# Performance work log

Hardware: AMD Instinct MI355X
Metric: run time of the kernel (lower is better)

Reference implementation:

```python
import jax, jax.numpy as jnp
import numpy as np
import math

N, E, D, R, L = 20000, 640000, 128, 16, 3
R_MAX = math.sqrt(2.0)
CENTERS = jnp.linspace(0.0, R_MAX, R)          # GaussianRBF centers on [0, sqrt(2)]
GAMMA = 1.0 / (2.0 * (R_MAX / (R - 1)) ** 2)   # 1/(2*sigma^2), sigma = center spacing


def _mlp(x, w1, b1, w2, b2):
    # mlp([din, d_h, dout]): Linear -> SiLU -> Linear (dropout=0.0)
    return jax.nn.silu(x @ w1 + b1) @ w2 + b2


def _ln(x, g, b):
    mu = jnp.mean(x, axis=-1, keepdims=True)
    v = jnp.var(x, axis=-1, keepdims=True)
    return (x - mu) * jax.lax.rsqrt(v + 1e-5) * g + b


def _time_emb(t):
    # SinusoidalEmbedding(dim=D)
    half = D // 2
    freqs = jnp.exp(-math.log(10000.0) * jnp.arange(half, dtype=jnp.float32) / (half - 1))
    a = t * freqs
    return jnp.concatenate([jnp.sin(a), jnp.cos(a)])


def setup_inputs():
    key = jax.random.key(0)
    ks = jax.random.split(key, 16)
    s = 0.05
    p = {}
    p["x_t"] = jax.random.normal(ks[0], (N, 3), dtype=jnp.float32)
    p["edge_index"] = jax.random.randint(ks[1], (2, E), 0, N)
    p["t"] = 25
    p["time_w1"] = jax.random.normal(ks[2], (D, D)) * s
    p["time_b1"] = jnp.zeros((D,))
    p["time_w2"] = jax.random.normal(ks[3], (D, D)) * s
    p["time_b2"] = jnp.zeros((D,))
    p["nodein_w1"] = jax.random.normal(ks[4], (3 + D, D)) * s
    p["nodein_b1"] = jnp.zeros((D,))
    p["nodein_w2"] = jax.random.normal(ks[5], (D, D)) * s
    p["nodein_b2"] = jnp.zeros((D,))
    p["phim_w1"] = jax.random.normal(ks[6], (L, 2 * D + R, D)) * s
    p["phim_b1"] = jnp.zeros((L, D))
    p["phim_w2"] = jax.random.normal(ks[7], (L, D, D)) * s
    p["phim_b2"] = jnp.zeros((L, D))
    p["phih_w1"] = jax.random.normal(ks[8], (L, 2 * D, D)) * s
    p["phih_b1"] = jnp.zeros((L, D))
    p["phih_w2"] = jax.random.normal(ks[9], (L, D, D)) * s
    p["phih_b2"] = jnp.zeros((L, D))
    p["ln_g"] = jnp.ones((L, D))
    p["ln_b"] = jnp.zeros((L, D))
    p["out_w1"] = jax.random.normal(ks[10], (D, D)) * s
    p["out_b1"] = jnp.zeros((D,))
    p["out_w2"] = jax.random.normal(ks[11], (D, 3)) * s
    p["out_b2"] = jnp.zeros((3,))
    return p


def reference(x_t, edge_index, t,
              time_w1, time_b1, time_w2, time_b2,
              nodein_w1, nodein_b1, nodein_w2, nodein_b2,
              phim_w1, phim_b1, phim_w2, phim_b2,
              phih_w1, phih_b1, phih_w2, phih_b2,
              ln_g, ln_b,
              out_w1, out_b1, out_w2, out_b2):
    # GraphDenoiser.forward: one denoiser call of the diffusion sampling loop.
    n = x_t.shape[0]
    src, dst = edge_index[0], edge_index[1]

    te = _mlp(_time_emb(jnp.asarray(t, jnp.float32)), time_w1, time_b1, time_w2, time_b2)
    h = _mlp(jnp.concatenate([x_t, jnp.broadcast_to(te, (n, D))], axis=-1),
             nodein_w1, nodein_b1, nodein_w2, nodein_b2)

    # edge geometry is fixed across layers (depends only on x_t)
    dx = x_t[src, :2] - x_t[dst, :2]                     # [E, 2]
    r = jnp.sqrt(jnp.sum(dx * dx, axis=-1) + 1e-8)       # [E]
    rbf = jnp.exp(-GAMMA * (r[:, None] - CENTERS) ** 2)  # [E, R]

    for i in range(L):  # WeightedInvariantMPNNLayer x L (edge_weight == 1)
        m_in = jnp.concatenate([h[src], h[dst], rbf], axis=-1)      # [E, 2D+R]
        m = _mlp(m_in, phim_w1[i], phim_b1[i], phim_w2[i], phim_b2[i])
        agg = jax.ops.segment_sum(m, dst, num_segments=n)           # scatter_sum
        h_up = _mlp(jnp.concatenate([h, agg], axis=-1),
                    phih_w1[i], phih_b1[i], phih_w2[i], phih_b2[i])
        h = _ln(h + h_up, ln_g[i], ln_b[i])

    return _mlp(h, out_w1, out_b1, out_w2, out_b2)  # predicted eps, [N, 3]
```

## Files before the change

### kernel.cpp

```cpp
#include <hip/hip_runtime.h>

typedef unsigned short u16;
typedef unsigned int u32;

#define NNODES 20000
#define NEDGES 640000
#define RBF_GAMMA 56.25f
#define SQRT2 1.4142135623730951f
#define PITCH 132
#define BPITCH 136

typedef __bf16 bf16x8 __attribute__((ext_vector_type(8)));
typedef float f32x4 __attribute__((ext_vector_type(4)));

__device__ __forceinline__ float b2f(u16 u) {
    union { float f; u32 i; } x; x.i = ((u32)u) << 16; return x.f;
}
__device__ __forceinline__ float hi2f(u32 w) {
    union { float f; u32 i; } x; x.i = w & 0xffff0000u; return x.f;
}
__device__ __forceinline__ float lo2f(u32 w) {
    union { float f; u32 i; } x; x.i = w << 16; return x.f;
}
__device__ __forceinline__ u16 f2b(float f) {
    union { float f; u32 i; } x; x.f = f;
    u32 r = (x.i + 0x7fffu + ((x.i >> 16) & 1u)) >> 16;
    return (u16)r;
}
__device__ __forceinline__ float silu(float v) {
    return v * __builtin_amdgcn_rcpf(1.0f + __expf(-v));
}
__device__ __forceinline__ void fma4(float4 w, float4 s, float& acc) {
    acc = fmaf(w.x, s.x, acc);
    acc = fmaf(w.y, s.y, acc);
    acc = fmaf(w.z, s.z, acc);
    acc = fmaf(w.w, s.w, acc);
}

__global__ __launch_bounds__(256) void k_hist(const int* __restrict__ ei, int* __restrict__ hist) {
    int e = blockIdx.x * 256 + threadIdx.x;
    atomicAdd(&hist[ei[NEDGES + e]], 1);
}

__global__ __launch_bounds__(1024) void k_scan(const int* __restrict__ hist,
                                               int* __restrict__ row_ptr,
                                               int* __restrict__ cursor) {
    __shared__ int psum[1024];
    int t = threadIdx.x;
    int base = t * 20;
    int s = 0;
    if (base < NNODES)
        for (int i = 0; i < 20; ++i) s += hist[base + i];
    psum[t] = s;
    __syncthreads();
    for (int off = 1; off < 1024; off <<= 1) {
        int v = (t >= off) ? psum[t - off] : 0;
        __syncthreads();
        psum[t] += v;
        __syncthreads();
    }
    int excl = psum[t] - s;
    if (base < NNODES) {
        int run = excl;
        for (int i = 0; i < 20; ++i) {
            row_ptr[base + i] = run;
            cursor[base + i] = run;
            run += hist[base + i];
        }
    }
    if (t == 1023) row_ptr[NNODES] = psum[1023];
}

__global__ __launch_bounds__(256) void k_scatter(const int* __restrict__ ei, int* __restrict__ cursor,
                                                 int* __restrict__ ssrc, int* __restrict__ sdst) {
    int e = blockIdx.x * 256 + threadIdx.x;
    int d = ei[NEDGES + e];
    int pos = atomicAdd(&cursor[d], 1);
    ssrc[pos] = ei[e];
    sdst[pos] = d;
}

__global__ __launch_bounds__(256) void k_prep_wr(const float* __restrict__ pmw1,
                                                 const float* __restrict__ pmb1,
                                                 u16* __restrict__ Wr) {
    int id = blockIdx.x * 256 + threadIdx.x;
    if (id >= 1536) return;
    int l = id / 512; int r = id - l * 512;
    int nt = r >> 6, lane = r & 63;
    int col = nt * 16 + (lane & 15);
    alignas(16) u16 tmp[8];
    #pragma unroll
    for (int jj = 0; jj < 8; ++jj) {
        int kk = (lane >> 4) * 8 + jj;
        float v = 0.f;
        if (kk < 16) v = pmw1[l * 34816 + (256 + kk) * 128 + col];
        else if (kk == 16) v = pmb1[l * 128 + col];
        tmp[jj] = f2b(v);
    }
    *(uint4*)(Wr + (size_t)id * 8) = *(const uint4*)tmp;
}

__global__ __launch_bounds__(256) void k_prep_yw(const float* __restrict__ pmw1,
                                                 u16* __restrict__ Yw) {
    int id = blockIdx.x * 256 + threadIdx.x;
    if (id >= 12288) return;
    int lane = id & 63;
    int g = id >> 6;
    int nt = g & 7; g >>= 3;
    int kc = g & 3; g >>= 2;
    int mat = g & 1; int l = g >> 1;
    int col = nt * 16 + (lane & 15);
    int kb = kc * 32 + ((lane >> 4) & 3) * 8;
    alignas(16) u16 tmp[8];
    #pragma unroll
    for (int jj = 0; jj < 8; ++jj)
        tmp[jj] = f2b(pmw1[(size_t)l * 34816 + (mat * 128 + kb + jj) * 128 + col]);
    *(uint4*)(Yw + (size_t)id * 8) = *(const uint4*)tmp;
}

struct PackM { const float* s[11]; float* d[11]; int K[11]; };
__global__ __launch_bounds__(256) void k_pack(PackM pm) {
    int m = blockIdx.y;
    int idx = blockIdx.x * 256 + threadIdx.x;
    if (idx >= pm.K[m] * 128) return;
    int k = idx >> 7, j = idx & 127;
    pm.d[m][(k >> 2) * 512 + j * 4 + (k & 3)] = pm.s[m][idx];
}

__global__ __launch_bounds__(256) void k_prep_m(const float* __restrict__ pmw2,
        const float* __restrict__ pmb2, const float* __restrict__ V1p,
        float* __restrict__ Mp, float* __restrict__ bvv) {
    const int l = blockIdx.y, bx = blockIdx.x;
    const float* V1 = V1p + (size_t)l * 32768;
    const int tid = threadIdx.x;
    const int w = tid >> 6, lane = tid & 63;
    const int cg = lane & 15, ng = lane >> 4;
    const int jc0 = w * 32 + cg * 2, jc1 = jc0 + 1;
    __shared__ alignas(16) float W2L[16][PITCH];
    __shared__ float b2L[128];
    if (bx < 8) {
        const float4* src = (const float4*)(pmw2 + (size_t)l * 16384 + bx * 16 * 128);
        for (int q = tid; q < 512; q += 256) {
            int row = q >> 5, part = q & 31;
            *(float4*)&W2L[row][part * 4] = src[q];
        }
        __syncthreads();
        int r0 = ng * 4;
        float acc[4][2];
        #pragma unroll
        for (int n = 0; n < 4; ++n) { acc[n][0] = 0.f; acc[n][1] = 0.f; }
        for (int mm = 0; mm < 32; ++mm) {
            float4 wa = *(const float4*)(V1 + (32 + mm) * 512 + jc0 * 4);
            float4 wb = *(const float4*)(V1 + (32 + mm) * 512 + jc1 * 4);
            #pragma unroll
            for (int n = 0; n < 4; ++n) {
                float4 s4 = *(const float4*)&W2L[r0 + n][mm * 4];
                fma4(wa, s4, acc[n][0]);
                fma4(wb, s4, acc[n][1]);
            }
        }
        #pragma unroll
        for (int n = 0; n < 4; ++n) {
            int kg = bx * 16 + r0 + n;
            Mp[(size_t)l * 16384 + (kg >> 2) * 512 + jc0 * 4 + (kg & 3)] = acc[n][0];
            Mp[(size_t)l * 16384 + (kg >> 2) * 512 + jc1 * 4 + (kg & 3)] = acc[n][1];
        }
    } else {
        if (tid < 128) b2L[tid] = pmb2[l * 128 + tid];
        __syncthreads();
        if (ng == 0) {
            float a0 = 0.f, a1 = 0.f;
            for (int mm = 0; mm < 32; ++mm) {
                float4 wa = *(const float4*)(V1 + (32 + mm) * 512 + jc0 * 4);
                float4 wb = *(const float4*)(V1 + (32 + mm) * 512 + jc1 * 4);
                float4 s4 = *(const float4*)&b2L[mm * 4];
                fma4(wa, s4, a0);
                fma4(wb, s4, a1);
            }
            bvv[l * 128 + jc0] = a0;
            bvv[l * 128 + jc1] = a1;
        }
    }
}

__global__ __launch_bounds__(128) void k_time(const int* __restrict__ tptr,
        const float* __restrict__ tw1, const float* __restrict__ tb1,
        const float* __restrict__ tw2, const float* __restrict__ tb2,
        const float* __restrict__ nw1, const float* __restrict__ nb1,
        float* __restrict__ base1) {
    __shared__ float emb[128], hid[128], te[128];
    int j = threadIdx.x;
    int raw = tptr[0];
    float tv;
    if (raw >= 0 && raw < (1 << 24)) tv = (float)raw;
    else tv = __int_as_float(raw);
    float fr = expf(-9.210340371976184f * (float)(j & 63) / 63.0f);
    float a = tv * fr;
    emb[j] = (j < 64) ? sinf(a) : cosf(a);
    __syncthreads();
    float acc = tb1[j];
    for (int k = 0; k < 128; ++k) acc += emb[k] * tw1[k * 128 + j];
    hid[j] = silu(acc);
    __syncthreads();
    acc = tb2[j];
    for (int k = 0; k < 128; ++k) acc += hid[k] * tw2[k * 128 + j];
    te[j] = acc;
    __syncthreads();
    acc = nb1[j];
    for (int k = 0; k < 128; ++k) acc += te[k] * nw1[(3 + k) * 128 + j];
    base1[j] = acc;
}

__global__ __launch_bounds__(256) void k_h0(const float* __restrict__ x, const float* __restrict__ base1,
        const float* __restrict__ nw1, const float* __restrict__ nw2p, const float* __restrict__ nb2,
        const u16* __restrict__ Yw,
        float* __restrict__ hf, u16* __restrict__ Ysrc, u16* __restrict__ Ydst) {
    const int tid = threadIdx.x;
    const int w = tid >> 6, lane = tid & 63;
    const int cg = lane & 15, ng = lane >> 4;
    const int jc0 = w * 32 + cg * 2, jc1 = jc0 + 1;
    const int n0 = ng * 4;
    const int base = blockIdx.x * 16;
    __shared__ alignas(16) float xl[16][4];
    __shared__ alignas(16) float hid[16][PITCH];
    __shared__ alignas(16) u16 hb16[16 * BPITCH];
    if (tid < 48) { int n = tid / 3, cc = tid - n * 3; xl[n][cc] = x[(size_t)(base + n) * 3 + cc]; }
    __syncthreads();
    {
        float w0a = nw1[jc0], w0b = nw1[jc1];
        float w1a = nw1[128 + jc0], w1b = nw1[128 + jc1];
        float w2a = nw1[256 + jc0], w2b = nw1[256 + jc1];
        float ba = base1[jc0], bb = base1[jc1];
        #pragma unroll
        for (int n = 0; n < 4; ++n) {
            int row = n0 + n;
            float x0 = xl[row][0], x1 = xl[row][1], x2 = xl[row][2];
            float2 v;
            v.x = silu(ba + x0 * w0a + x1 * w1a + x2 * w2a);
            v.y = silu(bb + x0 * w0b + x1 * w1b + x2 * w2b);
            *(float2*)&hid[row][jc0] = v;
        }
    }
    __syncthreads();
    float acc[4][2];
    {
        float ba = nb2[jc0], bb = nb2[jc1];
        #pragma unroll
        for (int n = 0; n < 4; ++n) { acc[n][0] = ba; acc[n][1] = bb; }
        for (int kk = 0; kk < 32; ++kk) {
            float4 wa = *(const float4*)(nw2p + kk * 512 + jc0 * 4);
            float4 wb = *(const float4*)(nw2p + kk * 512 + jc1 * 4);
            #pragma unroll
            for (int n = 0; n < 4; ++n) {
                float4 s4 = *(const float4*)&hid[n0 + n][kk * 4];
                fma4(wa, s4, acc[n][0]);
                fma4(wb, s4, acc[n][1]);
            }
        }
    }
    __syncthreads();
    #pragma unroll
    for (int n = 0; n < 4; ++n) {
        int row = n0 + n;
        *(float2*)&hf[(size_t)(base + row) * 128 + jc0] = make_float2(acc[n][0], acc[n][1]);
        *(u32*)&hb16[row * BPITCH + jc0] = (u32)f2b(acc[n][0]) | ((u32)f2b(acc[n][1]) << 16);
    }
    __syncthreads();
    {
        const int mat = w >> 1, half = w & 1;
        const int lrow = lane & 15, quad = lane >> 4;
        bf16x8 a[4];
        #pragma unroll
        for (int kc = 0; kc < 4; ++kc)
            a[kc] = *(const bf16x8*)(hb16 + lrow * BPITCH + kc * 32 + quad * 8);
        u16* dst = mat ? Ydst : Ysrc;
        #pragma unroll
        for (int t = 0; t < 4; ++t) {
            int nt = half * 4 + t;
            f32x4 a4 = {0.f, 0.f, 0.f, 0.f};
            #pragma unroll
            for (int kc = 0; kc < 4; ++kc) {
                bf16x8 b = *(const bf16x8*)(Yw + (size_t)(((mat * 4 + kc) * 8 + nt) * 512 + lane * 8));
                a4 = __builtin_amdgcn_mfma_f32_16x16x32_bf16(a[kc], b, a4, 0, 0, 0);
            }
            #pragma unroll
            for (int r = 0; r < 4; ++r)
                dst[(size_t)(base + quad * 4 + r) * 128 + nt * 16 + lrow] = f2b(a4[r]);
        }
    }
}

__global__ __launch_bounds__(512, 8) void k_edge(
        const u16* __restrict__ Ysrc, const u16* __restrict__ Ydst,
        const float* __restrict__ x,
        const int* __restrict__ ssrc, const int* __restrict__ sdst,
        const u16* __restrict__ Wr,
        float* __restrict__ s_glob) {
    __shared__ alignas(16) u16 sst[128 * 72];
    __shared__ alignas(16) u16 ys[64 * 128];
    __shared__ float rv[64];
    __shared__ int s_d[65];
    __shared__ int s_s[64];
    const int tid = threadIdx.x;
    const int e0 = blockIdx.x * 64;
    if (tid < 64) {
        int s = ssrc[e0 + tid], d = sdst[e0 + tid];
        s_s[tid] = s; s_d[tid] = d;
        float ddx = x[s * 3] - x[d * 3];
        float ddy = x[s * 3 + 1] - x[d * 3 + 1];
        rv[tid] = sqrtf(ddx * ddx + ddy * ddy + 1e-8f);
    } else if (tid == 64) {
        s_d[64] = -1;
    }
    __syncthreads();
    #pragma unroll
    for (int i = 0; i < 2; ++i) {
        int cch = tid + i * 512;
        int e = cch >> 4, part = cch & 15;
        *(uint4*)(ys + e * 128 + part * 8) = *(const uint4*)(Ysrc + (size_t)s_s[e] * 128 + part * 8);
    }
    const int w = tid >> 6, lane = tid & 63;
    const int m = w & 3, nh = w >> 2;
    const int lrow = lane & 15, quad = lane >> 4;
    float r = rv[m * 16 + lrow];
    union { bf16x8 v; u16 u[8]; } af;
    #pragma unroll
    for (int j = 0; j < 8; ++j) {
        int kk = quad * 8 + j;
        float v;
        if (kk < 16) {
            float dd = r - SQRT2 * (float)kk / 15.0f;
            v = __expf(-RBF_GAMMA * dd * dd);
        } else v = (kk == 16) ? 1.0f : 0.0f;
        af.u[j] = f2b(v);
    }
    {
        const u16* Bp = Wr + lane * 8;
        #pragma unroll
        for (int t = 0; t < 4; ++t) {
            int nt = nh * 4 + t;
            f32x4 a4 = {0.f, 0.f, 0.f, 0.f};
            bf16x8 b = *(const bf16x8*)(Bp + nt * 512);
            a4 = __builtin_amdgcn_mfma_f32_16x16x32_bf16(af.v, b, a4, 0, 0, 0);
            int col = nt * 16 + lrow;
            u32 lo = (u32)f2b(a4[0]) | ((u32)f2b(a4[1]) << 16);
            u32 hi = (u32)f2b(a4[2]) | ((u32)f2b(a4[3]) << 16);
            *(uint2*)(sst + col * 72 + m * 16 + quad * 4) = make_uint2(lo, hi);
        }
    }
    __syncthreads();
    {
        const int col = tid & 127, q = tid >> 7;
        const int r0 = q * 16;
        float a = 0.f;
        int cd = s_d[r0];
        float yd = b2f(Ydst[(size_t)cd * 128 + col]);
        #pragma unroll
        for (int h = 0; h < 2; ++h) {
            uint4 c0 = *(const uint4*)(sst + col * 72 + r0 + h * 8);
            float sv8[8];
            sv8[0] = lo2f(c0.x); sv8[1] = hi2f(c0.x);
            sv8[2] = lo2f(c0.y); sv8[3] = hi2f(c0.y);
            sv8[4] = lo2f(c0.z); sv8[5] = hi2f(c0.z);
            sv8[6] = lo2f(c0.w); sv8[7] = hi2f(c0.w);
            #pragma unroll
            for (int i = 0; i < 8; ++i) {
                int rr = r0 + h * 8 + i;
                int nd = s_d[rr + 1];
                float v = sv8[i] + b2f(ys[rr * 128 + col]) + yd;
                a += silu(v);
                bool last = (h == 1 && i == 7);
                if (last || nd != cd) {
                    atomicAdd(&s_glob[(size_t)cd * 128 + col], a);
                    a = 0.f;
                    if (!last && nd != cd)
                        yd = b2f(Ydst[(size_t)nd * 128 + col]);
                }
                cd = nd;
            }
        }
    }
}

__global__ __launch_bounds__(256) void k_node(float* __restrict__ s_glob, const int* __restrict__ row_ptr,
        float* __restrict__ hf,
        const float* __restrict__ Mp, const float* __restrict__ V1p, const float* __restrict__ V2p,
        const float* __restrict__ bv, const float* __restrict__ c1, const float* __restrict__ c2,
        const float* __restrict__ lng, const float* __restrict__ lnb,
        const u16* __restrict__ Yw,
        u16* __restrict__ Ysrc, u16* __restrict__ Ydst) {
    const int tid = threadIdx.x;
    const int w = tid >> 6, lane = tid & 63;
    const int cg = lane & 15, ng = lane >> 4;
    const int jc0 = w * 32 + cg * 2, jc1 = jc0 + 1;
    const int n0 = ng * 4;
    const int base = blockIdx.x * 16;
    __shared__ alignas(16) float sv[16][PITCH], hv[16][PITCH];
    __shared__ alignas(16) u16 ybf[16 * BPITCH];
    __shared__ float mv[16][2];
    __shared__ int rp[17];
    float (*uv)[PITCH] = sv;
    float (*xs)[PITCH] = sv;

    if (tid < 17) rp[tid] = row_ptr[base + tid];
    {
        const float4* sg4 = (const float4*)(s_glob + (size_t)base * 128);
        float4* sg4w = (float4*)(s_glob + (size_t)base * 128);
        const float4* hg4 = (const float4*)(hf + (size_t)base * 128);
        for (int q = tid; q < 512; q += 256) {
            int row = q >> 5, part = q & 31;
            *(float4*)&sv[row][part * 4] = sg4[q];
            *(float4*)&hv[row][part * 4] = hg4[q];
            sg4w[q] = make_float4(0.f, 0.f, 0.f, 0.f);
        }
    }
    __syncthreads();

    float acc[4][2];
    {
        float ba = c1[jc0], bb = c1[jc1];
        float bva = bv[jc0], bvb = bv[jc1];
        #pragma unroll
        for (int n = 0; n < 4; ++n) {
            float dg = (float)(rp[n0 + n + 1] - rp[n0 + n]);
            acc[n][0] = ba + dg * bva; acc[n][1] = bb + dg * bvb;
        }
        for (int kk = 0; kk < 32; ++kk) {
            float4 wa = *(const float4*)(V1p + kk * 512 + jc0 * 4);
            float4 wb = *(const float4*)(V1p + kk * 512 + jc1 * 4);
            #pragma unroll
            for (int n = 0; n < 4; ++n) {
                float4 s4 = *(const float4*)&hv[n0 + n][kk * 4];
                fma4(wa, s4, acc[n][0]);
                fma4(wb, s4, acc[n][1]);
            }
        }
        for (int kk = 0; kk < 32; ++kk) {
            float4 wa = *(const float4*)(Mp + kk * 512 + jc0 * 4);
            float4 wb = *(const float4*)(Mp + kk * 512 + jc1 * 4);
            #pragma unroll
            for (int n = 0; n < 4; ++n) {
                float4 s4 = *(const float4*)&sv[n0 + n][kk * 4];
                fma4(wa, s4, acc[n][0]);
                fma4(wb, s4, acc[n][1]);
            }
        }
    }
    __syncthreads();
    #pragma unroll
    for (int n = 0; n < 4; ++n)
        *(float2*)&uv[n0 + n][jc0] = make_float2(silu(acc[n][0]), silu(acc[n][1]));
    __syncthreads();
    {
        float ba = c2[jc0], bb = c2[jc1];
        #pragma unroll
        for (int n = 0; n < 4; ++n) { acc[n][0] = ba; acc[n][1] = bb; }
        for (int kk = 0; kk < 32; ++kk) {
            float4 wa = *(const float4*)(V2p + kk * 512 + jc0 * 4);
            float4 wb = *(const float4*)(V2p + kk * 512 + jc1 * 4);
            #pragma unroll
            for (int n = 0; n < 4; ++n) {
                float4 s4 = *(const float4*)&uv[n0 + n][kk * 4];
                fma4(wa, s4, acc[n][0]);
                fma4(wb, s4, acc[n][1]);
            }
        }
        #pragma unroll
        for (int n = 0; n < 4; ++n) {
            float2 h2 = *(const float2*)&hv[n0 + n][jc0];
            acc[n][0] += h2.x; acc[n][1] += h2.y;
        }
    }
    __syncthreads();
    #pragma unroll
    for (int n = 0; n < 4; ++n)
        *(float2*)&xs[n0 + n][jc0] = make_float2(acc[n][0], acc[n][1]);
    __syncthreads();
    {
        int row = tid >> 4, part = tid & 15;
        float4 a = *(const float4*)&xs[row][part * 8];
        float4 b = *(const float4*)&xs[row][part * 8 + 4];
        float s1 = a.x + a.y + a.z + a.w + b.x + b.y + b.z + b.w;
        float s2 = a.x * a.x + a.y * a.y + a.z * a.z + a.w * a.w
                 + b.x * b.x + b.y * b.y + b.z * b.z + b.w * b.w;
        #pragma unroll
        for (int mq = 1; mq < 16; mq <<= 1) {
            s1 += __shfl_xor(s1, mq, 64);
            s2 += __shfl_xor(s2, mq, 64);
        }
        if (part == 0) { mv[row][0] = s1; mv[row][1] = s2; }
    }
    __syncthreads();
    {
        float ga = lng[jc0], gb = lng[jc1];
        float bba = lnb[jc0], bbb = lnb[jc1];
        #pragma unroll
        for (int n = 0; n < 4; ++n) {
            int row = n0 + n;
            float mu = mv[row][0] * (1.0f / 128.0f);
            float var = mv[row][1] * (1.0f / 128.0f) - mu * mu;
            float rs = rsqrtf(var + 1e-5f);
            float y0 = (xs[row][jc0] - mu) * rs * ga + bba;
            float y1 = (xs[row][jc1] - mu) * rs * gb + bbb;
            *(float2*)&hf[(size_t)(base + row) * 128 + jc0] = make_float2(y0, y1);
            *(u32*)&ybf[row * BPITCH + jc0] = (u32)f2b(y0) | ((u32)f2b(y1) << 16);
        }
    }
    if (Yw != nullptr) {
        __syncthreads();
        const int mat = w >> 1, half = w & 1;
        const int lrow = lane & 15, quad = lane >> 4;
        bf16x8 a[4];
        #pragma unroll
        for (int kc = 0; kc < 4; ++kc)
            a[kc] = *(const bf16x8*)(ybf + lrow * BPITCH + kc * 32 + quad * 8);
        u16* dst = mat ? Ydst : Ysrc;
        #pragma unroll
        for (int t = 0; t < 4; ++t) {
            int nt = half * 4 + t;
            f32x4 a4 = {0.f, 0.f, 0.f, 0.f};
            #pragma unroll
            for (int kc = 0; kc < 4; ++kc) {
                bf16x8 b = *(const bf16x8*)(Yw + (size_t)(((mat * 4 + kc) * 8 + nt) * 512 + lane * 8));
                a4 = __builtin_amdgcn_mfma_f32_16x16x32_bf16(a[kc], b, a4, 0, 0, 0);
            }
            #pragma unroll
            for (int r = 0; r < 4; ++r)
                dst[(size_t)(base + quad * 4 + r) * 128 + nt * 16 + lrow] = f2b(a4[r]);
        }
    }
}

__global__ __launch_bounds__(256) void k_out(const float* __restrict__ hf, const float* __restrict__ ow1p,
        const float* __restrict__ ob1, const float* __restrict__ ow2, const float* __restrict__ ob2,
        float* __restrict__ out) {
    const int tid = threadIdx.x;
    const int w = tid >> 6, lane = tid & 63;
    const int cg = lane & 15, ng = lane >> 4;
    const int jc0 = w * 32 + cg * 2, jc1 = jc0 + 1;
    const int n0 = ng * 4;
    const int base = blockIdx.x * 16;
    __shared__ alignas(16) float hv[16][PITCH];
    __shared__ float hid[16][PITCH];
    for (int q = tid; q < 512; q += 256) {
        int row = q >> 5, part = q & 31;
        *(float4*)&hv[row][part * 4] = ((const float4*)(hf + (size_t)base * 128))[q];
    }
    __syncthreads();
    float acc[4][2];
    {
        float ba = ob1[jc0], bb = ob1[jc1];
        #pragma unroll
        for (int n = 0; n < 4; ++n) { acc[n][0] = ba; acc[n][1] = bb; }
    }
    for (int kk = 0; kk < 32; ++kk) {
        float4 wa = *(const float4*)(ow1p + kk * 512 + jc0 * 4);
        float4 wb = *(const float4*)(ow1p + kk * 512 + jc1 * 4);
        #pragma unroll
        for (int n = 0; n < 4; ++n) {
            float4 s4 = *(const float4*)&hv[n0 + n][kk * 4];
            fma4(wa, s4, acc[n][0]);
            fma4(wb, s4, acc[n][1]);
        }
    }
    #pragma unroll
    for (int n = 0; n < 4; ++n) {
        hid[n0 + n][jc0] = silu(acc[n][0]);
        hid[n0 + n][jc1] = silu(acc[n][1]);
    }
    __syncthreads();
    if (tid < 48) {
        int n = tid / 3, cc = tid - n * 3;
        float o = ob2[cc];
        for (int k = 0; k < 128; ++k) o += hid[n][k] * ow2[k * 3 + cc];
        out[(size_t)(base + n) * 3 + cc] = o;
    }
}

extern "C" void kernel_launch(void* const* d_in, const int* in_sizes, int n_in,
                              void* d_out, int out_size, void* d_ws, size_t ws_size,
                              hipStream_t stream) {
    const float* x    = (const float*)d_in[0];
    const int* ei     = (const int*)d_in[1];
    const int* tptr   = (const int*)d_in[2];
    const float* tw1  = (const float*)d_in[3];
    const float* tb1  = (const float*)d_in[4];
    const float* tw2  = (const float*)d_in[5];
    const float* tb2  = (const float*)d_in[6];
    const float* nw1  = (const float*)d_in[7];
    const float* nb1  = (const float*)d_in[8];
    const float* nw2  = (const float*)d_in[9];
    const float* nb2  = (const float*)d_in[10];
    const float* pmw1 = (const float*)d_in[11];
    const float* pmb1 = (const float*)d_in[12];
    const float* pmw2 = (const float*)d_in[13];
    const float* pmb2 = (const float*)d_in[14];
    const float* phw1 = (const float*)d_in[15];
    const float* phb1 = (const float*)d_in[16];
    const float* phw2 = (const float*)d_in[17];
    const float* phb2 = (const float*)d_in[18];
    const float* lng  = (const float*)d_in[19];
    const float* lnb  = (const float*)d_in[20];
    const float* ow1  = (const float*)d_in[21];
    const float* ob1  = (const float*)d_in[22];
    const float* ow2  = (const float*)d_in[23];
    const float* ob2  = (const float*)d_in[24];
    float* out = (float*)d_out;

    char* wsp = (char*)d_ws;
    size_t off = 0;
    auto alloc = [&](size_t bytes) -> void* {
        void* p = wsp + off;
        off += (bytes + 255) & ~(size_t)255;
        return p;
    };
    int* hist    = (int*)alloc((size_t)NNODES * 4);
    int* cursor  = (int*)alloc((size_t)NNODES * 4);
    int* row_ptr = (int*)alloc((size_t)(NNODES + 1) * 4);
    int* ssrc    = (int*)alloc((size_t)NEDGES * 4);
    int* sdst    = (int*)alloc((size_t)NEDGES * 4);
    u16* Wr      = (u16*)alloc((size_t)3 * 8 * 64 * 8 * 2);
    u16* Yw      = (u16*)alloc((size_t)3 * 2 * 4 * 8 * 64 * 8 * 2);
    float* base1 = (float*)alloc(128 * 4);
    float* V1p   = (float*)alloc((size_t)3 * 256 * 128 * 4);
    float* V2p   = (float*)alloc((size_t)3 * 128 * 128 * 4);
    float* nw2p  = (float*)alloc((size_t)128 * 128 * 4);
    float* ow1p  = (float*)alloc((size_t)128 * 128 * 4);
    float* W2p   = (float*)alloc((size_t)3 * 128 * 128 * 4);
    float* Mp    = (float*)alloc((size_t)3 * 128 * 128 * 4);
    float* bvv   = (float*)alloc((size_t)3 * 128 * 4);
    float* hf    = (float*)alloc((size_t)NNODES * 128 * 4);
    u16* Ysrc    = (u16*)alloc((size_t)NNODES * 128 * 2);
    u16* Ydst    = (u16*)alloc((size_t)NNODES * 128 * 2);
    float* s_glob= (float*)alloc((size_t)NNODES * 128 * 4);

    (void)hipMemsetAsync(hist, 0, (size_t)NNODES * 4, stream);
    k_hist<<<NEDGES / 256, 256, 0, stream>>>(ei, hist);
    k_scan<<<1, 1024, 0, stream>>>(hist, row_ptr, cursor);
    k_scatter<<<NEDGES / 256, 256, 0, stream>>>(ei, cursor, ssrc, sdst);
    k_prep_wr<<<6, 256, 0, stream>>>(pmw1, pmb1, Wr);
    k_prep_yw<<<48, 256, 0, stream>>>(pmw1, Yw);

    PackM pm;
    for (int l = 0; l < 3; ++l) {
        pm.s[l] = pmw2 + (size_t)l * 16384;      pm.d[l] = W2p + (size_t)l * 16384;  pm.K[l] = 128;
        pm.s[3 + l] = phw2 + (size_t)l * 16384;  pm.d[3 + l] = V2p + (size_t)l * 16384; pm.K[3 + l] = 128;
        pm.s[6 + l] = phw1 + (size_t)l * 32768;  pm.d[6 + l] = V1p + (size_t)l * 32768; pm.K[6 + l] = 256;
    }
    pm.s[9] = nw2;  pm.d[9] = nw2p;  pm.K[9] = 128;
    pm.s[10] = ow1; pm.d[10] = ow1p; pm.K[10] = 128;
    k_pack<<<dim3(128, 11), 256, 0, stream>>>(pm);
    k_prep_m<<<dim3(9, 3), 256, 0, stream>>>(pmw2, pmb2, V1p, Mp, bvv);

    k_time<<<1, 128, 0, stream>>>(tptr, tw1, tb1, tw2, tb2, nw1, nb1, base1);
    k_h0<<<1250, 256, 0, stream>>>(x, base1, nw1, nw2p, nb2, Yw, hf, Ysrc, Ydst);

    (void)hipMemsetAsync(s_glob, 0, (size_t)NNODES * 128 * 4, stream);
    for (int l = 0; l < 3; ++l) {
        k_edge<<<NEDGES / 64, 512, 0, stream>>>(Ysrc, Ydst, x, ssrc, sdst,
                Wr + (size_t)l * 4096, s_glob);
        const u16* YwN = (l < 2) ? (Yw + (size_t)(l + 1) * 32768) : nullptr;
        k_node<<<1250, 256, 0, stream>>>(s_glob, row_ptr, hf,
                Mp + (size_t)l * 16384, V1p + (size_t)l * 32768, V2p + (size_t)l * 16384,
                bvv + l * 128, phb1 + l * 128, phb2 + l * 128, lng + l * 128, lnb + l * 128,
                YwN, Ysrc, Ydst);
    }
    k_out<<<1250, 256, 0, stream>>>(hf, ow1p, ob1, ow2, ob2, out);
}
```

Measured before the change: 573.1 us.

## Fuse edge epilogue into MFMA registers, dropping the shared-memory staging pass

```diff
diff --git a/kernel.cpp b/kernel.cpp
--- a/kernel.cpp
+++ b/kernel.cpp
@@ -15,12 +15,6 @@
 
 __device__ __forceinline__ float b2f(u16 u) {
     union { float f; u32 i; } x; x.i = ((u32)u) << 16; return x.f;
-}
-__device__ __forceinline__ float hi2f(u32 w) {
-    union { float f; u32 i; } x; x.i = w & 0xffff0000u; return x.f;
-}
-__device__ __forceinline__ float lo2f(u32 w) {
-    union { float f; u32 i; } x; x.i = w << 16; return x.f;
 }
 __device__ __forceinline__ u16 f2b(float f) {
     union { float f; u32 i; } x; x.f = f;
@@ -296,10 +290,9 @@
         const int* __restrict__ ssrc, const int* __restrict__ sdst,
         const u16* __restrict__ Wr,
         float* __restrict__ s_glob) {
-    __shared__ alignas(16) u16 sst[128 * 72];
-    __shared__ alignas(16) u16 ys[64 * 128];
+    __shared__ alignas(16) u16 ys[64 * BPITCH];
     __shared__ float rv[64];
-    __shared__ int s_d[65];
+    __shared__ int s_d[64];
     __shared__ int s_s[64];
     const int tid = threadIdx.x;
     const int e0 = blockIdx.x * 64;
@@ -309,15 +302,13 @@
         float ddx = x[s * 3] - x[d * 3];
         float ddy = x[s * 3 + 1] - x[d * 3 + 1];
         rv[tid] = sqrtf(ddx * ddx + ddy * ddy + 1e-8f);
-    } else if (tid == 64) {
-        s_d[64] = -1;
     }
     __syncthreads();
     #pragma unroll
     for (int i = 0; i < 2; ++i) {
         int cch = tid + i * 512;
         int e = cch >> 4, part = cch & 15;
-        *(uint4*)(ys + e * 128 + part * 8) = *(const uint4*)(Ysrc + (size_t)s_s[e] * 128 + part * 8);
+        *(uint4*)(ys + e * BPITCH + part * 8) = *(const uint4*)(Ysrc + (size_t)s_s[e] * 128 + part * 8);
     }
     const int w = tid >> 6, lane = tid & 63;
     const int m = w & 3, nh = w >> 2;
@@ -334,49 +325,32 @@
         } else v = (kk == 16) ? 1.0f : 0.0f;
         af.u[j] = f2b(v);
     }
-    {
-        const u16* Bp = Wr + lane * 8;
-        #pragma unroll
-        for (int t = 0; t < 4; ++t) {
-            int nt = nh * 4 + t;
-            f32x4 a4 = {0.f, 0.f, 0.f, 0.f};
-            bf16x8 b = *(const bf16x8*)(Bp + nt * 512);
-            a4 = __builtin_amdgcn_mfma_f32_16x16x32_bf16(af.v, b, a4, 0, 0, 0);
-            int col = nt * 16 + lrow;
-            u32 lo = (u32)f2b(a4[0]) | ((u32)f2b(a4[1]) << 16);
-            u32 hi = (u32)f2b(a4[2]) | ((u32)f2b(a4[3]) << 16);
-            *(uint2*)(sst + col * 72 + m * 16 + quad * 4) = make_uint2(lo, hi);
-        }
-    }
-    __syncthreads();
-    {
-        const int col = tid & 127, q = tid >> 7;
-        const int r0 = q * 16;
-        float a = 0.f;
-        int cd = s_d[r0];
-        float yd = b2f(Ydst[(size_t)cd * 128 + col]);
-        #pragma unroll
-        for (int h = 0; h < 2; ++h) {
-            uint4 c0 = *(const uint4*)(sst + col * 72 + r0 + h * 8);
-            float sv8[8];
-            sv8[0] = lo2f(c0.x); sv8[1] = hi2f(c0.x);
-            sv8[2] = lo2f(c0.y); sv8[3] = hi2f(c0.y);
-            sv8[4] = lo2f(c0.z); sv8[5] = hi2f(c0.z);
-            sv8[6] = lo2f(c0.w); sv8[7] = hi2f(c0.w);
-            #pragma unroll
-            for (int i = 0; i < 8; ++i) {
-                int rr = r0 + h * 8 + i;
-                int nd = s_d[rr + 1];
-                float v = sv8[i] + b2f(ys[rr * 128 + col]) + yd;
-                a += silu(v);
-                bool last = (h == 1 && i == 7);
-                if (last || nd != cd) {
-                    atomicAdd(&s_glob[(size_t)cd * 128 + col], a);
-                    a = 0.f;
-                    if (!last && nd != cd)
-                        yd = b2f(Ydst[(size_t)nd * 128 + col]);
-                }
-                cd = nd;
+    __syncthreads();
+    const int R = m * 16 + quad * 4;
+    const int d0 = s_d[R], d3 = s_d[R + 3];
+    const u16* Bp = Wr + lane * 8;
+    #pragma unroll
+    for (int t = 0; t < 4; ++t) {
+        int nt = nh * 4 + t;
+        f32x4 a4 = {0.f, 0.f, 0.f, 0.f};
+        bf16x8 b = *(const bf16x8*)(Bp + nt * 512);
+        a4 = __builtin_amdgcn_mfma_f32_16x16x32_bf16(af.v, b, a4, 0, 0, 0);
+        int col = nt * 16 + lrow;
+        if (d0 == d3) {
+            float yd = b2f(Ydst[(size_t)d0 * 128 + col]);
+            float s = 0.f;
+            #pragma unroll
+            for (int i2 = 0; i2 < 4; ++i2) {
+                float v = a4[i2] + b2f(ys[(R + i2) * BPITCH + col]) + yd;
+                s += silu(v);
+            }
+            atomicAdd(&s_glob[(size_t)d0 * 128 + col], s);
+        } else {
+            #pragma unroll
+            for (int i2 = 0; i2 < 4; ++i2) {
+                int di = s_d[R + i2];
+                float v = a4[i2] + b2f(ys[(R + i2) * BPITCH + col]) + b2f(Ydst[(size_t)di * 128 + col]);
+                atomicAdd(&s_glob[(size_t)di * 128 + col], silu(v));
             }
         }
     }
```

New measurement: 1.065 ms. 1.86x slower.
